# Kernel optimization log

Hardware: AMD Instinct MI355X
Metric: run time of the kernel (lower is better)

The kernel has to match this reference:

```python
import jax, jax.numpy as jnp
import numpy as np

FG_THRESH = 0.5
BG_HI = 0.5
BG_LO = 0.0
CLS_LAMBDA = 1.0
BBOX2D_LAMBDA = 1.0
BBOX3D_LAMBDA = 1.0

A, FH, FW, STRIDE = 36, 32, 106, 16  # 36*32*106 = 122112 anchors
B, G, NC = 4, 64, 4


def _smooth_l1(x):
    ax = jnp.abs(x)
    return jnp.where(ax < 1.0, 0.5 * ax * ax, ax - 0.5)


def setup_inputs() -> dict:
    rng = np.random.RandomState(0)
    # anchors: [x1,y1,x2,y2, z, w3d, h3d, l3d, ry], centered at origin
    ws = rng.uniform(16, 256, A).astype(np.float32)
    hs = rng.uniform(16, 256, A).astype(np.float32)
    anchors = np.zeros((A, 9), np.float32)
    anchors[:, 0] = -ws / 2; anchors[:, 1] = -hs / 2
    anchors[:, 2] = ws / 2;  anchors[:, 3] = hs / 2
    anchors[:, 4] = rng.uniform(5, 50, A)
    anchors[:, 5:8] = rng.uniform(1, 5, (A, 3))
    anchors[:, 8] = rng.uniform(-np.pi, np.pi, A)
    # rois = anchors tiled over the feature grid (locate_anchors), col 4 = anchor idx
    sx, sy = np.meshgrid(np.arange(FW) * STRIDE, np.arange(FH) * STRIDE)
    shifts = np.stack([sx.ravel(), sy.ravel(), sx.ravel(), sy.ravel()], 1).astype(np.float32)
    N = FH * FW * A
    rois = np.zeros((N, 5), np.float32)
    rois[:, :4] = (shifts[:, None, :] + anchors[None, :, :4]).reshape(-1, 4)
    rois[:, 4] = np.tile(np.arange(A), FH * FW)
    # GT 2D boxes (x1,y1,x2,y2) inside the 1696x512 image
    gcx = rng.uniform(0, FW * STRIDE, (B, G)); gcy = rng.uniform(0, FH * STRIDE, (B, G))
    gw = rng.uniform(30, 200, (B, G)); gh = rng.uniform(30, 200, (B, G))
    gt_boxes = np.stack([gcx - gw / 2, gcy - gh / 2, gcx + gw / 2, gcy + gh / 2], -1).astype(np.float32)
    # GT 3D: projected 3D center (u,v), z, w3d, h3d, l3d, ry
    gt_boxes_3d = np.stack([
        gcx, gcy,
        rng.uniform(5, 50, (B, G)),
        rng.uniform(1, 5, (B, G)), rng.uniform(1, 5, (B, G)), rng.uniform(1, 5, (B, G)),
        rng.uniform(-np.pi, np.pi, (B, G)),
    ], -1).astype(np.float32)
    gt_labels = rng.randint(1, NC, (B, G)).astype(np.int32)
    bbox_means = (rng.randn(1, 11) * 0.01).astype(np.float32)
    bbox_stds = (0.1 + rng.rand(1, 11) * 0.2).astype(np.float32)
    key = jax.random.key(0)
    k1, k2, k3, k4 = jax.random.split(key, 4)
    return {
        "cls": jax.random.normal(k1, (B, N, NC), jnp.float32),
        "prob": jax.random.uniform(k2, (B, N, NC), jnp.float32),
        "bbox_2d": 0.1 * jax.random.normal(k3, (B, N, 4), jnp.float32),
        "bbox_3d": 0.1 * jax.random.normal(k4, (B, N, 7), jnp.float32),
        "rois": jnp.asarray(rois),
        "anchors": jnp.asarray(anchors),
        "bbox_means": jnp.asarray(bbox_means),
        "bbox_stds": jnp.asarray(bbox_stds),
        "gt_boxes": jnp.asarray(gt_boxes),
        "gt_boxes_3d": jnp.asarray(gt_boxes_3d),
        "gt_labels": jnp.asarray(gt_labels),
    }


def _loss(cls, prob, bbox_2d, bbox_3d, rois, anchors, bbox_means, bbox_stds,
          gt_boxes, gt_boxes_3d, gt_labels):
    # anchor geometry (the +1.0 convention matches the torch code)
    widths = rois[:, 2] - rois[:, 0] + 1.0          # [N]
    heights = rois[:, 3] - rois[:, 1] + 1.0
    ctr_x = rois[:, 0] + 0.5 * widths
    ctr_y = rois[:, 1] + 0.5 * heights
    aidx = rois[:, 4].astype(jnp.int32)
    src = anchors[aidx]                             # [N,9] gathered anchors

    # IoU between every roi and every GT: [B,N,G]
    rx1 = rois[None, :, None, 0]; ry1 = rois[None, :, None, 1]
    rx2 = rois[None, :, None, 2]; ry2 = rois[None, :, None, 3]
    gx1 = gt_boxes[:, None, :, 0]; gy1 = gt_boxes[:, None, :, 1]
    gx2 = gt_boxes[:, None, :, 2]; gy2 = gt_boxes[:, None, :, 3]
    iw = jnp.clip(jnp.minimum(rx2, gx2) - jnp.maximum(rx1, gx1) + 1.0, 0.0)
    ih = jnp.clip(jnp.minimum(ry2, gy2) - jnp.maximum(ry1, gy1) + 1.0, 0.0)
    inter = iw * ih
    area_r = (rx2 - rx1 + 1.0) * (ry2 - ry1 + 1.0)
    area_g = (gx2 - gx1 + 1.0) * (gy2 - gy1 + 1.0)
    ols = inter / (area_r + area_g - inter)         # [B,N,G]

    best_iou = jnp.max(ols, axis=-1)                # [B,N]
    best_gt = jnp.argmax(ols, axis=-1)              # [B,N]

    fg = best_iou >= FG_THRESH
    bg = (best_iou < BG_HI) & (best_iou >= BG_LO) & (~fg)

    matched_lbl = jnp.take_along_axis(gt_labels, best_gt, axis=1)   # [B,N]
    labels = jnp.where(fg, matched_lbl, 0)

    gb = jnp.take_along_axis(gt_boxes, best_gt[..., None], axis=1)  # [B,N,4]
    gw = gb[..., 2] - gb[..., 0] + 1.0
    gh = gb[..., 3] - gb[..., 1] + 1.0
    gcx = gb[..., 0] + 0.5 * gw
    gcy = gb[..., 1] + 0.5 * gh
    t2d = jnp.stack([
        (gcx - ctr_x) / widths,
        (gcy - ctr_y) / heights,
        jnp.log(gw / widths),
        jnp.log(gh / heights),
    ], -1)
    t2d = (t2d - bbox_means[0, 0:4]) / bbox_stds[0, 0:4]

    g3 = jnp.take_along_axis(gt_boxes_3d, best_gt[..., None], axis=1)  # [B,N,7]
    t3d = jnp.stack([
        (g3[..., 0] - ctr_x) / widths,
        (g3[..., 1] - ctr_y) / heights,
        g3[..., 2] - src[:, 4],
        jnp.log(g3[..., 3] / src[:, 5]),
        jnp.log(g3[..., 4] / src[:, 6]),
        jnp.log(g3[..., 5] / src[:, 7]),
        g3[..., 6] - src[:, 8],
    ], -1)
    t3d = (t3d - bbox_means[0, 4:11]) / bbox_stds[0, 4:11]

    # ---- losses
    w_fg = fg.astype(cls.dtype)
    n_fg = jnp.maximum(jnp.sum(w_fg), 1.0)
    loss_b2d = jnp.sum(jnp.sum(_smooth_l1(bbox_2d - t2d), -1) * w_fg) / n_fg
    loss_b3d = jnp.sum(jnp.sum(_smooth_l1(bbox_3d - t3d), -1) * w_fg) / n_fg

    w_cls = (fg | bg).astype(cls.dtype)
    logp = jax.nn.log_softmax(cls, axis=-1)
    ce = -jnp.take_along_axis(logp, labels[..., None], axis=-1)[..., 0]
    loss_cls = jnp.sum(ce * w_cls) / jnp.maximum(jnp.sum(w_cls), 1.0)

    return CLS_LAMBDA * loss_cls + BBOX2D_LAMBDA * loss_b2d + BBOX3D_LAMBDA * loss_b3d


def reference(cls, prob, bbox_2d, bbox_3d, rois, anchors, bbox_means, bbox_stds,
              gt_boxes, gt_boxes_3d, gt_labels):
    return _loss(cls, prob, bbox_2d, bbox_3d, rois, anchors, bbox_means, bbox_stds,
                 gt_boxes, gt_boxes_3d, gt_labels)
```

## Files before the change

### kernel.cpp

```cpp
#include <hip/hip_runtime.h>
#include <math.h>

#define AA 36
#define FWW 106
#define NTOT 122112
#define BB 4
#define GG 64
#define STRIDE_PX 16

constexpr int BLOCK = 512;
constexpr int NW    = BLOCK / 64;
constexpr int BLOCKS_PER_B = (NTOT + BLOCK - 1) / BLOCK;
constexpr int NBLK = BB * BLOCKS_PER_B;

__device__ __forceinline__ float smooth_l1(float x) {
    float ax = fabsf(x);
    return (ax < 1.0f) ? 0.5f * ax * ax : ax - 0.5f;
}
__device__ __forceinline__ float frcp(float x) { return __builtin_amdgcn_rcpf(x); }

#define DPP_ZERO(x, ctrl, rm)                                                 \
    __int_as_float(__builtin_amdgcn_update_dpp(0, __float_as_int(x),          \
                   ctrl, rm, 0xf, true))
#define RLANE_F(v, l) __int_as_float(__builtin_amdgcn_readlane(__float_as_int(v), (l)))

__device__ __forceinline__ float wave_sum64(float x) {
    x += DPP_ZERO(x, 0x111, 0xf);
    x += DPP_ZERO(x, 0x112, 0xf);
    x += DPP_ZERO(x, 0x114, 0xf);
    x += DPP_ZERO(x, 0x118, 0xf);
    x += DPP_ZERO(x, 0x142, 0xa);
    x += DPP_ZERO(x, 0x143, 0xc);
    return x;
}

__global__ __launch_bounds__(BLOCK) void rpn_loss_main(
    const float* __restrict__ cls,
    const float* __restrict__ bbox2d,
    const float* __restrict__ bbox3d,
    const float* __restrict__ anchors,
    const float* __restrict__ means,
    const float* __restrict__ stds,
    const float* __restrict__ gt_boxes,
    const float* __restrict__ gt3d,
    const int*   __restrict__ gt_labels,
    float4* __restrict__ part)
{
    __shared__ float4 s_gt4[GG];
    __shared__ float  s_gS[GG];
    __shared__ int    s_gidx[GG];
    __shared__ float4 s_anch4[AA];
    __shared__ float  s_anch[AA * 13];
    __shared__ unsigned long long s_bal[NW];
    __shared__ float4 s_red[NW];
    __shared__ int    s_K;

    const int tid  = threadIdx.x;
    const int lane = tid & 63;
    const int wv   = tid >> 6;
    const int wvu  = __builtin_amdgcn_readfirstlane(wv);
    const int b    = blockIdx.x / BLOCKS_PER_B;
    const int bpos = blockIdx.x % BLOCKS_PER_B;
    const int n0   = bpos * BLOCK;
    const int n    = n0 + tid;
    const bool valid = (n < NTOT);

    const float4* __restrict__ gtb = reinterpret_cast<const float4*>(gt_boxes) + b * GG;

    const size_t row = (size_t)b * NTOT + n;
    float4 c = make_float4(0.f, 0.f, 0.f, 0.f);
    if (valid) c = reinterpret_cast<const float4*>(cls)[row];

    if (tid < AA) {
        float a[9];
        #pragma unroll
        for (int k = 0; k < 9; ++k) a[k] = anchors[tid * 9 + k];
        #pragma unroll
        for (int k = 0; k < 9; ++k) s_anch[tid * 13 + k] = a[k];
        s_anch4[tid] = make_float4(a[0], a[1], a[2] - a[0] + 1.0f, a[3] - a[1] + 1.0f);
    }

    const int nlast = (n0 + BLOCK - 1 < NTOT) ? (n0 + BLOCK - 1) : (NTOT - 1);
    const int s0  = n0 / AA,  s1  = nlast / AA;
    const int sy0 = s0 / FWW, sy1 = s1 / FWW;
    float fxA0, fxA1, fyA, fxB0, fxB1, fyB;
    if (sy0 == sy1) {
        fxA0 = (float)((s0 % FWW) * STRIDE_PX); fxA1 = (float)((s1 % FWW) * STRIDE_PX);
        fyA  = (float)(sy0 * STRIDE_PX);
        fxB0 = fxA0; fxB1 = fxA1; fyB = fyA;
    } else {
        fxA0 = (float)((s0 % FWW) * STRIDE_PX); fxA1 = (float)((FWW - 1) * STRIDE_PX);
        fyA  = (float)(sy0 * STRIDE_PX);
        fxB0 = 0.0f;                            fxB1 = (float)((s1 % FWW) * STRIDE_PX);
        fyB  = (float)(sy1 * STRIDE_PX);
    }

    const float4 gt   = gtb[lane];
    const float  gz1p = gt.z + 1.0f;
    const float  gw1p = gt.w + 1.0f;
    const float  ag   = (gz1p - gt.x) * (gw1p - gt.y);

    bool pass = false;
    for (int a = wvu; a < AA; a += NW) {
        const float ax1 = anchors[a * 9 + 0];
        const float ay1 = anchors[a * 9 + 1];
        const float aw  = anchors[a * 9 + 2] - ax1 + 1.0f;
        const float ah  = anchors[a * 9 + 3] - ay1 + 1.0f;
        const float thr = aw * ah + ag;
        float iwA = fminf(fxA1 + ax1 + aw, gz1p) - fmaxf(fxA0 + ax1, gt.x);
        float ihA = fminf(fyA  + ay1 + ah, gw1p) - fmaxf(fyA  + ay1, gt.y);
        iwA = fmaxf(fminf(iwA, aw), 0.0f);
        ihA = fmaxf(fminf(ihA, ah), 0.0f);
        pass |= (3.0f * iwA * ihA >= thr);
        float iwB = fminf(fxB1 + ax1 + aw, gz1p) - fmaxf(fxB0 + ax1, gt.x);
        float ihB = fminf(fyB  + ay1 + ah, gw1p) - fmaxf(fyB  + ay1, gt.y);
        iwB = fmaxf(fminf(iwB, aw), 0.0f);
        ihB = fmaxf(fminf(ihB, ah), 0.0f);
        pass |= (3.0f * iwB * ihB >= thr);
    }
    const unsigned long long wmask = __ballot(pass);
    if (lane == 0) s_bal[wv] = wmask;
    __syncthreads();

    if (wv == 0) {
        unsigned long long mask = 0ull;
        #pragma unroll
        for (int j = 0; j < NW; ++j) mask |= s_bal[j];
        if ((mask >> lane) & 1ull) {
            const int pos = __popcll(mask & ((1ull << lane) - 1ull));
            s_gt4[pos]  = make_float4(gt.x, gt.y, gz1p, gw1p);
            s_gS[pos]   = ag;
            s_gidx[pos] = lane;
        }
        if (lane == 0) s_K = __popcll(mask);
    }
    __syncthreads();

    const float4 sv4 = s_gt4[lane];
    const float  svS = s_gS[lane];

    const int aidx  = n % AA;
    const int shift = n / AA;
    const float sx  = (float)((shift % FWW) * STRIDE_PX);
    const float sy  = (float)((shift / FWW) * STRIDE_PX);
    const float4 A4 = s_anch4[aidx];
    const float aw  = A4.z;
    const float ah  = A4.w;
    const float x1  = sx + A4.x;
    const float y1  = sy + A4.y;
    const float x2p = x1 + aw;
    const float y2p = y1 + ah;
    const float ar  = aw * ah;

    const float lse = __logf(__expf(c.x) + __expf(c.y) + __expf(c.z) + __expf(c.w));

    const int K = s_K;
    float bi = 0.0f, bS = 1.0f;
    int   bk = 0;
    for (int k = 0; k < K; ++k) {
        const float gxs = RLANE_F(sv4.x, k);
        const float gys = RLANE_F(sv4.y, k);
        const float gzs = RLANE_F(sv4.z, k);
        const float gws = RLANE_F(sv4.w, k);
        const float ags = RLANE_F(svS,   k);
        const float iw = fminf(x2p, gzs) - fmaxf(x1, gxs);
        const float ih = fmaxf(fminf(y2p, gws) - fmaxf(y1, gys), 0.0f);
        const float inter = iw * ih;
        const float S     = ar + ags;
        const bool upd = inter * bS > bi * S;
        bi = upd ? inter : bi;
        bS = upd ? S     : bS;
        bk = upd ? k     : bk;
    }
    const bool fg = valid && (3.0f * bi >= bS);

    int label = 0;
    if (fg) label = gt_labels[b * GG + s_gidx[bk]];
    const float csel = (label == 0) ? c.x : (label == 1) ? c.y :
                       (label == 2) ? c.z : c.w;
    const float ce = valid ? (lse - csel) : 0.0f;

    float l23 = 0.0f;
    if (fg) {
        const float cx  = x1 + 0.5f * aw;
        const float cy  = y1 + 0.5f * ah;
        const float rw  = frcp(aw);
        const float rh  = frcp(ah);
        const float4 gq = s_gt4[bk];
        const float gw_ = gq.z - gq.x;
        const float gh_ = gq.w - gq.y;
        const float gcx = gq.x + 0.5f * gw_;
        const float gcy = gq.y + 0.5f * gh_;
        float t2[4];
        t2[0] = (gcx - cx) * rw;
        t2[1] = (gcy - cy) * rh;
        t2[2] = __logf(gw_ * rw);
        t2[3] = __logf(gh_ * rh);
        const float4 p2 = reinterpret_cast<const float4*>(bbox2d)[row];
        const float p2a[4] = {p2.x, p2.y, p2.z, p2.w};
        #pragma unroll
        for (int k = 0; k < 4; ++k)
            l23 += smooth_l1(p2a[k] - (t2[k] - means[k]) * frcp(stds[k]));

        const float* an = &s_anch[aidx * 13];
        const float* g3 = gt3d + ((size_t)b * GG + s_gidx[bk]) * 7;
        float t3[7];
        t3[0] = (g3[0] - cx) * rw;
        t3[1] = (g3[1] - cy) * rh;
        t3[2] = g3[2] - an[4];
        t3[3] = __logf(g3[3] * frcp(an[5]));
        t3[4] = __logf(g3[4] * frcp(an[6]));
        t3[5] = __logf(g3[5] * frcp(an[7]));
        t3[6] = g3[6] - an[8];
        const float* p3 = bbox3d + row * 7;
        #pragma unroll
        for (int k = 0; k < 7; ++k)
            l23 += smooth_l1(p3[k] - (t3[k] - means[4 + k]) * frcp(stds[4 + k]));
    }

    const float vce = wave_sum64(ce);
    const float vl  = wave_sum64(l23);
    const float nfgw = (float)__popcll(__ballot(fg));
    if (lane == 63) s_red[wv] = make_float4(vce, vl, nfgw, 0.f);
    __syncthreads();
    if (tid < NW) {
        float4 p = s_red[tid];
        #pragma unroll
        for (int m = 1; m < NW; m <<= 1) {
            p.x += __shfl_xor(p.x, m, 64);
            p.y += __shfl_xor(p.y, m, 64);
            p.z += __shfl_xor(p.z, m, 64);
        }
        if (tid == 0) part[blockIdx.x] = p;
    }
}

__global__ __launch_bounds__(256) void rpn_loss_fin(
    const float4* __restrict__ part, float* __restrict__ out)
{
    __shared__ float4 sh[4];
    float ce = 0.f, l23 = 0.f, nfg = 0.f;
    for (int i = threadIdx.x; i < NBLK; i += 256) {
        const float4 p = part[i];
        ce += p.x; l23 += p.y; nfg += p.z;
    }
    ce  = wave_sum64(ce);
    l23 = wave_sum64(l23);
    nfg = wave_sum64(nfg);
    const int lane = threadIdx.x & 63;
    const int wv   = threadIdx.x >> 6;
    if (lane == 63) sh[wv] = make_float4(ce, l23, nfg, 0.f);
    __syncthreads();
    if (threadIdx.x == 0) {
        float a = 0.f, l = 0.f, g = 0.f;
        #pragma unroll
        for (int i = 0; i < 4; ++i) { a += sh[i].x; l += sh[i].y; g += sh[i].z; }
        out[0] = a / (float)((size_t)BB * NTOT) + l / fmaxf(g, 1.0f);
    }
}

extern "C" void kernel_launch(void* const* d_in, const int* in_sizes, int n_in,
                              void* d_out, int out_size, void* d_ws, size_t ws_size,
                              hipStream_t stream) {
    const float* cls     = (const float*)d_in[0];
    const float* bbox2d  = (const float*)d_in[2];
    const float* bbox3d  = (const float*)d_in[3];
    const float* anchors = (const float*)d_in[5];
    const float* means   = (const float*)d_in[6];
    const float* stds    = (const float*)d_in[7];
    const float* gtb     = (const float*)d_in[8];
    const float* gt3     = (const float*)d_in[9];
    const int*   glbl    = (const int*)d_in[10];
    float4* part = (float4*)d_ws;
    float*  out  = (float*)d_out;

    rpn_loss_main<<<dim3(NBLK), BLOCK, 0, stream>>>(cls, bbox2d, bbox3d, anchors,
                                                    means, stds, gtb, gt3, glbl, part);
    rpn_loss_fin<<<1, 256, 0, stream>>>(part, out);
}
```

Measured before the change: 16.02 us.

## Move per-block GT pruning into a separate pre-pass kernel

The per-block candidate GT pruning (ballot over anchors crossed with GT boxes) moves out of the main kernel into a new rpn_prune kernel that writes one 64-bit mask per block to workspace. The main kernel reads its mask, computes K with popcount, and drops one barrier and the in-block ballot combine. The cost is an extra kernel launch plus a round trip of the masks through global memory, and each prune wave now loops over all 36 anchors serially.

```diff
diff --git a/kernel.cpp b/kernel.cpp
--- a/kernel.cpp
+++ b/kernel.cpp
@@ -12,6 +12,8 @@
 constexpr int NW    = BLOCK / 64;
 constexpr int BLOCKS_PER_B = (NTOT + BLOCK - 1) / BLOCK;
 constexpr int NBLK = BB * BLOCKS_PER_B;
+constexpr int PR_BLOCK = 512;
+constexpr int PR_GRID  = (NBLK * 64 + PR_BLOCK - 1) / PR_BLOCK;
 
 __device__ __forceinline__ float smooth_l1(float x) {
     float ax = fabsf(x);
@@ -34,56 +36,13 @@
     return x;
 }
 
-__global__ __launch_bounds__(BLOCK) void rpn_loss_main(
-    const float* __restrict__ cls,
-    const float* __restrict__ bbox2d,
-    const float* __restrict__ bbox3d,
-    const float* __restrict__ anchors,
-    const float* __restrict__ means,
-    const float* __restrict__ stds,
-    const float* __restrict__ gt_boxes,
-    const float* __restrict__ gt3d,
-    const int*   __restrict__ gt_labels,
-    float4* __restrict__ part)
+__device__ __forceinline__ void block_windows(int n0,
+    float& fxA0, float& fxA1, float& fyA,
+    float& fxB0, float& fxB1, float& fyB)
 {
-    __shared__ float4 s_gt4[GG];
-    __shared__ float  s_gS[GG];
-    __shared__ int    s_gidx[GG];
-    __shared__ float4 s_anch4[AA];
-    __shared__ float  s_anch[AA * 13];
-    __shared__ unsigned long long s_bal[NW];
-    __shared__ float4 s_red[NW];
-    __shared__ int    s_K;
-
-    const int tid  = threadIdx.x;
-    const int lane = tid & 63;
-    const int wv   = tid >> 6;
-    const int wvu  = __builtin_amdgcn_readfirstlane(wv);
-    const int b    = blockIdx.x / BLOCKS_PER_B;
-    const int bpos = blockIdx.x % BLOCKS_PER_B;
-    const int n0   = bpos * BLOCK;
-    const int n    = n0 + tid;
-    const bool valid = (n < NTOT);
-
-    const float4* __restrict__ gtb = reinterpret_cast<const float4*>(gt_boxes) + b * GG;
-
-    const size_t row = (size_t)b * NTOT + n;
-    float4 c = make_float4(0.f, 0.f, 0.f, 0.f);
-    if (valid) c = reinterpret_cast<const float4*>(cls)[row];
-
-    if (tid < AA) {
-        float a[9];
-        #pragma unroll
-        for (int k = 0; k < 9; ++k) a[k] = anchors[tid * 9 + k];
-        #pragma unroll
-        for (int k = 0; k < 9; ++k) s_anch[tid * 13 + k] = a[k];
-        s_anch4[tid] = make_float4(a[0], a[1], a[2] - a[0] + 1.0f, a[3] - a[1] + 1.0f);
-    }
-
     const int nlast = (n0 + BLOCK - 1 < NTOT) ? (n0 + BLOCK - 1) : (NTOT - 1);
     const int s0  = n0 / AA,  s1  = nlast / AA;
     const int sy0 = s0 / FWW, sy1 = s1 / FWW;
-    float fxA0, fxA1, fyA, fxB0, fxB1, fyB;
     if (sy0 == sy1) {
         fxA0 = (float)((s0 % FWW) * STRIDE_PX); fxA1 = (float)((s1 % FWW) * STRIDE_PX);
         fyA  = (float)(sy0 * STRIDE_PX);
@@ -94,14 +53,30 @@
         fxB0 = 0.0f;                            fxB1 = (float)((s1 % FWW) * STRIDE_PX);
         fyB  = (float)(sy1 * STRIDE_PX);
     }
-
-    const float4 gt   = gtb[lane];
-    const float  gz1p = gt.z + 1.0f;
-    const float  gw1p = gt.w + 1.0f;
-    const float  ag   = (gz1p - gt.x) * (gw1p - gt.y);
+}
+
+__global__ __launch_bounds__(PR_BLOCK) void rpn_prune(
+    const float* __restrict__ anchors,
+    const float* __restrict__ gt_boxes,
+    unsigned long long* __restrict__ masks)
+{
+    const int gthread = blockIdx.x * PR_BLOCK + threadIdx.x;
+    const int vb   = gthread >> 6;
+    const int lane = threadIdx.x & 63;
+    if (vb >= NBLK) return;
+
+    const int b    = vb / BLOCKS_PER_B;
+    const int bpos = vb % BLOCKS_PER_B;
+    float fxA0, fxA1, fyA, fxB0, fxB1, fyB;
+    block_windows(bpos * BLOCK, fxA0, fxA1, fyA, fxB0, fxB1, fyB);
+
+    const float4 gt = reinterpret_cast<const float4*>(gt_boxes)[b * GG + lane];
+    const float gz1p = gt.z + 1.0f;
+    const float gw1p = gt.w + 1.0f;
+    const float ag   = (gz1p - gt.x) * (gw1p - gt.y);
 
     bool pass = false;
-    for (int a = wvu; a < AA; a += NW) {
+    for (int a = 0; a < AA; ++a) {
         const float ax1 = anchors[a * 9 + 0];
         const float ay1 = anchors[a * 9 + 1];
         const float aw  = anchors[a * 9 + 2] - ax1 + 1.0f;
@@ -118,21 +93,67 @@
         ihB = fmaxf(fminf(ihB, ah), 0.0f);
         pass |= (3.0f * iwB * ihB >= thr);
     }
-    const unsigned long long wmask = __ballot(pass);
-    if (lane == 0) s_bal[wv] = wmask;
-    __syncthreads();
+    const unsigned long long m = __ballot(pass);
+    if (lane == 0) masks[vb] = m;
+}
+
+__global__ __launch_bounds__(BLOCK) void rpn_loss_main(
+    const float* __restrict__ cls,
+    const float* __restrict__ bbox2d,
+    const float* __restrict__ bbox3d,
+    const float* __restrict__ anchors,
+    const float* __restrict__ means,
+    const float* __restrict__ stds,
+    const float* __restrict__ gt_boxes,
+    const float* __restrict__ gt3d,
+    const int*   __restrict__ gt_labels,
+    const unsigned long long* __restrict__ masks,
+    float4* __restrict__ part)
+{
+    __shared__ float4 s_gt4[GG];
+    __shared__ float  s_gS[GG];
+    __shared__ int    s_gidx[GG];
+    __shared__ float4 s_anch4[AA];
+    __shared__ float  s_anch[AA * 13];
+    __shared__ float4 s_red[NW];
+
+    const int tid  = threadIdx.x;
+    const int lane = tid & 63;
+    const int wv   = tid >> 6;
+    const int b    = blockIdx.x / BLOCKS_PER_B;
+    const int bpos = blockIdx.x % BLOCKS_PER_B;
+    const int n0   = bpos * BLOCK;
+    const int n    = n0 + tid;
+    const bool valid = (n < NTOT);
+
+    const float4* __restrict__ gtb = reinterpret_cast<const float4*>(gt_boxes) + b * GG;
+
+    const size_t row = (size_t)b * NTOT + n;
+    float4 c = make_float4(0.f, 0.f, 0.f, 0.f);
+    if (valid) c = reinterpret_cast<const float4*>(cls)[row];
+
+    const unsigned long long mask = masks[blockIdx.x];
+    const int K = __popcll(mask);
+
+    if (tid < AA) {
+        float a[9];
+        #pragma unroll
+        for (int k = 0; k < 9; ++k) a[k] = anchors[tid * 9 + k];
+        #pragma unroll
+        for (int k = 0; k < 9; ++k) s_anch[tid * 13 + k] = a[k];
+        s_anch4[tid] = make_float4(a[0], a[1], a[2] - a[0] + 1.0f, a[3] - a[1] + 1.0f);
+    }
 
     if (wv == 0) {
-        unsigned long long mask = 0ull;
-        #pragma unroll
-        for (int j = 0; j < NW; ++j) mask |= s_bal[j];
+        const float4 gt   = gtb[lane];
+        const float  gz1p = gt.z + 1.0f;
+        const float  gw1p = gt.w + 1.0f;
         if ((mask >> lane) & 1ull) {
             const int pos = __popcll(mask & ((1ull << lane) - 1ull));
             s_gt4[pos]  = make_float4(gt.x, gt.y, gz1p, gw1p);
-            s_gS[pos]   = ag;
+            s_gS[pos]   = (gz1p - gt.x) * (gw1p - gt.y);
             s_gidx[pos] = lane;
         }
-        if (lane == 0) s_K = __popcll(mask);
     }
     __syncthreads();
 
@@ -154,7 +175,6 @@
 
     const float lse = __logf(__expf(c.x) + __expf(c.y) + __expf(c.z) + __expf(c.w));
 
-    const int K = s_K;
     float bi = 0.0f, bS = 1.0f;
     int   bk = 0;
     for (int k = 0; k < K; ++k) {
@@ -271,10 +291,14 @@
     const float* gtb     = (const float*)d_in[8];
     const float* gt3     = (const float*)d_in[9];
     const int*   glbl    = (const int*)d_in[10];
+
     float4* part = (float4*)d_ws;
+    unsigned long long* masks = (unsigned long long*)(part + NBLK);
     float*  out  = (float*)d_out;
 
+    rpn_prune<<<dim3(PR_GRID), PR_BLOCK, 0, stream>>>(anchors, gtb, masks);
     rpn_loss_main<<<dim3(NBLK), BLOCK, 0, stream>>>(cls, bbox2d, bbox3d, anchors,
-                                                    means, stds, gtb, gt3, glbl, part);
+                                                    means, stds, gtb, gt3, glbl,
+                                                    masks, part);
     rpn_loss_fin<<<1, 256, 0, stream>>>(part, out);
 }
```

Result: slower. 21.24 us (+32.6%).
